# Performance work log

Hardware: AMD Instinct MI355X
Metric: run time of the kernel (lower is better)

The kernel has to match this reference:

```python
import jax, jax.numpy as jnp
import numpy as np

DIM = 768
NUM_HEADS = 12
HEAD_DIM = DIM // NUM_HEADS


def setup_inputs() -> dict:
    key = jax.random.key(0)
    k1, k2, k3 = jax.random.split(key, 3)
    B, N = 2, 2048
    x = jax.random.normal(k1, (B, N, DIM), dtype=jnp.float32)
    qkv_w = jax.random.normal(k2, (3 * DIM, DIM), dtype=jnp.float32) * 0.02
    proj_w = jax.random.normal(k3, (DIM, DIM), dtype=jnp.float32) * 0.02
    proj_b = jnp.zeros((DIM,), dtype=jnp.float32)
    freq_params = jnp.ones((NUM_HEADS, 1), dtype=jnp.float32) * 0.5  # Parameter init ones*0.5
    return {"x": x, "qkv_w": qkv_w, "proj_w": proj_w, "proj_b": proj_b,
            "freq_params": freq_params}


def _forward(x, qkv_w, proj_w, proj_b, freq_params):
    B, N, C = x.shape
    H, D = NUM_HEADS, HEAD_DIM
    scale = D ** (-0.5)
    # qkv projection -> (3, B, H, N, D)
    qkv = (x @ qkv_w.T).reshape(B, N, 3, H, D).transpose(2, 0, 3, 1, 4)
    q, k, v = qkv[0], qkv[1], qkv[2]
    # FFT along the token axis (axis=2 of [B,H,N,D])
    q_freq = jnp.fft.fft(q, axis=2)
    k_freq = jnp.fft.fft(k, axis=2)
    # Adaptive per-head low-pass: cutoff = int(N * sigmoid(freq_param)),
    # frequencies >= cutoff attenuated by exp(-(i - cutoff) / (N/4)).
    cutoff = jnp.floor(N * jax.nn.sigmoid(freq_params[:, 0]))        # (H,)
    idx = jnp.arange(N, dtype=jnp.float32)                            # (N,)
    rel = idx[None, :] - cutoff[:, None]                              # (H, N)
    atten = jnp.where(rel >= 0, jnp.exp(-rel / (N / 4.0)), 1.0)       # (H, N)
    atten = atten[None, :, :, None]                                   # (1, H, N, 1)
    q_filt = jnp.fft.ifft(q_freq * atten, axis=2).real
    k_filt = jnp.fft.ifft(k_freq * atten, axis=2).real
    # Attention
    attn = jnp.einsum('bhnd,bhmd->bhnm', q_filt, k_filt) * scale
    attn = jax.nn.softmax(attn, axis=-1)
    out = jnp.einsum('bhnm,bhmd->bhnd', attn, v)
    out = out.transpose(0, 2, 1, 3).reshape(B, N, C)
    return out @ proj_w.T + proj_b


def reference(x, qkv_w, proj_w, proj_b, freq_params):
    return _forward(x, qkv_w, proj_w, proj_b, freq_params)
```

## Files before the change

kernel.cpp:

```cpp
#include <hip/hip_runtime.h>
#include <math.h>

#define SEQ 2048
#define NH 12
#define HD 64
#define DIM 768

typedef _Float16 half_t;
typedef _Float16 f16x8 __attribute__((ext_vector_type(8)));
typedef _Float16 f16x4 __attribute__((ext_vector_type(4)));
typedef float f32x4 __attribute__((ext_vector_type(4)));

__device__ __forceinline__ void dma16(const half_t* g, half_t* l) {
  __builtin_amdgcn_global_load_lds(
      (const __attribute__((address_space(1))) unsigned int*)g,
      (__attribute__((address_space(3))) unsigned int*)l, 16, 0, 0);
}

__global__ __launch_bounds__(256) void cvt_f32_f16(
    const float* __restrict__ a, const float* __restrict__ b,
    const float* __restrict__ c, half_t* __restrict__ a16,
    half_t* __restrict__ b16, half_t* __restrict__ c16) {
  const size_t NA = 786432, NB = 442368;
  size_t i = (size_t)blockIdx.x * 256 + threadIdx.x;
  const float* src; half_t* dst; size_t off;
  if (i < NA) { src = a; dst = a16; off = i; }
  else if (i < NA + NB) { src = b; dst = b16; off = i - NA; }
  else { src = c; dst = c16; off = i - NA - NB; }
  float4 v = *(const float4*)&src[off * 4];
  f16x4 h;
  h[0] = (half_t)v.x; h[1] = (half_t)v.y; h[2] = (half_t)v.z; h[3] = (half_t)v.w;
  *(f16x4*)&dst[off * 4] = h;
}

__global__ __launch_bounds__(256) void gemm_qkv_f16(
    const half_t* __restrict__ x, const half_t* __restrict__ w,
    float* __restrict__ qT, float* __restrict__ kT, half_t* __restrict__ vb) {
  __shared__ half_t As[128][64];
  __shared__ half_t Bs[128][64];
  const int tid = threadIdx.x;
  const int lane = tid & 63, wave = tid >> 6;
  const int quad = lane >> 4, l16 = lane & 15;
  const int wr = wave >> 1, wc = wave & 1;
  const int row0 = blockIdx.y * 128;
  const int col0 = blockIdx.x * 128;
  const int srow = tid >> 3;
  const int schk = tid & 7;

  f32x4 acc[4][4] = {};

  for (int k0 = 0; k0 < DIM; k0 += 64) {
    f16x8 av[4], bv[4];
#pragma unroll
    for (int p = 0; p < 4; p++) {
      av[p] = *(const f16x8*)&x[(size_t)(row0 + srow + p * 32) * DIM + k0 + schk * 8];
      bv[p] = *(const f16x8*)&w[(size_t)(col0 + srow + p * 32) * DIM + k0 + schk * 8];
    }
    __syncthreads();
#pragma unroll
    for (int p = 0; p < 4; p++) {
      int r = srow + p * 32;
      int cs = ((schk ^ (r & 7)) << 3);
      *(f16x8*)&As[r][cs] = av[p];
      *(f16x8*)&Bs[r][cs] = bv[p];
    }
    __syncthreads();
#pragma unroll
    for (int ks = 0; ks < 2; ks++) {
      f16x8 af[4], bf[4];
#pragma unroll
      for (int i = 0; i < 4; i++) {
        int rr = wr * 64 + i * 16 + l16;
        af[i] = *(const f16x8*)&As[rr][((ks * 4 + quad) ^ (rr & 7)) << 3];
      }
#pragma unroll
      for (int j = 0; j < 4; j++) {
        int rr = wc * 64 + j * 16 + l16;
        bf[j] = *(const f16x8*)&Bs[rr][((ks * 4 + quad) ^ (rr & 7)) << 3];
      }
#pragma unroll
      for (int i = 0; i < 4; i++)
#pragma unroll
        for (int j = 0; j < 4; j++)
          acc[i][j] = __builtin_amdgcn_mfma_f32_16x16x32_f16(af[i], bf[j], acc[i][j], 0, 0, 0);
    }
  }

  const int fbase = col0 + wc * 64;
#pragma unroll
  for (int i = 0; i < 4; i++) {
    int n = row0 + wr * 64 + i * 16 + quad * 4;
    int b = n >> 11, nn = n & (SEQ - 1);
#pragma unroll
    for (int j = 0; j < 4; j++) {
      int f = fbase + j * 16 + l16;
      if (col0 < 1536) {
        float* dst = (col0 < 768) ? qT : kT;
        int fo = (col0 < 768) ? f : f - 768;
        *(f32x4*)&dst[((size_t)(b * 768 + fo)) * SEQ + nn] = acc[i][j];
      } else {
        int fo = f - 1536;
        int h = fo >> 6, d = fo & 63;
        int bh = b * NH + h;
        int ch = nn >> 6, cw = (nn & 63) >> 3, sub = nn & 7;
        f16x4 hv;
#pragma unroll
        for (int r = 0; r < 4; r++) hv[r] = (half_t)acc[i][j][r];
        *(f16x4*)&vb[((((size_t)bh * 32 + ch) * 64 + d) << 6) +
                     (((cw ^ (d & 7)) << 3) + sub)] = hv;
      }
    }
  }
}

__device__ __forceinline__ void fft2048_dif_fwd(float* re, float* im, int tid) {
  for (int M = 2048; M >= 8; M >>= 2) {
    const int q = M >> 2;
    const float ang = -6.283185307179586f / (float)M;
#pragma unroll 2
    for (int g = tid; g < 512; g += 256) {
      int j = g & (q - 1);
      int base = ((g & ~(q - 1)) << 2) | j;
      float s1, c1;
      __sincosf(ang * (float)j, &s1, &c1);
      float c2 = c1 * c1 - s1 * s1, s2 = 2.0f * c1 * s1;
      float Ar = re[base],         Ai = im[base];
      float Br = re[base + q],     Bi = im[base + q];
      float Cr = re[base + 2*q],   Ci = im[base + 2*q];
      float Dr = re[base + 3*q],   Di = im[base + 3*q];
      float A1r = Ar + Cr, A1i = Ai + Ci;
      float t1r = Ar - Cr, t1i = Ai - Ci;
      float C1r = c1 * t1r - s1 * t1i, C1i = c1 * t1i + s1 * t1r;
      float B1r = Br + Dr, B1i = Bi + Di;
      float t2r = Br - Dr, t2i = Bi - Di;
      float u2r = c1 * t2r - s1 * t2i, u2i = c1 * t2i + s1 * t2r;
      float D1r = u2i, D1i = -u2r;
      re[base]         = A1r + B1r; im[base]         = A1i + B1i;
      float t3r = A1r - B1r, t3i = A1i - B1i;
      re[base + q]     = c2 * t3r - s2 * t3i;
      im[base + q]     = c2 * t3i + s2 * t3r;
      re[base + 2*q]   = C1r + D1r; im[base + 2*q]   = C1i + D1i;
      float t4r = C1r - D1r, t4i = C1i - D1i;
      re[base + 3*q]   = c2 * t4r - s2 * t4i;
      im[base + 3*q]   = c2 * t4i + s2 * t4r;
    }
    __syncthreads();
  }
#pragma unroll 2
  for (int i = tid; i < 1024; i += 256) {
    float ar = re[2*i], ai = im[2*i], br = re[2*i+1], bi = im[2*i+1];
    re[2*i]   = ar + br; im[2*i]   = ai + bi;
    re[2*i+1] = ar - br; im[2*i+1] = ai - bi;
  }
  __syncthreads();
}

__device__ __forceinline__ void fft2048_dit_inv(float* re, float* im, int tid) {
  for (int L = 2; L <= 512; L <<= 2) {
    const int h = L >> 1;
    const float ang = 3.14159265358979f / (float)L;
#pragma unroll 2
    for (int g = tid; g < SEQ / 4; g += 256) {
      int p = g & (h - 1);
      int i0 = ((g & ~(h - 1)) << 2) | p;
      float s2, c2;
      __sincosf(ang * (float)p, &s2, &c2);
      float c1 = c2 * c2 - s2 * s2, s1 = 2.0f * c2 * s2;
      float ar = re[i0],         ai = im[i0];
      float br = re[i0 + h],     bi = im[i0 + h];
      float cr = re[i0 + L],     ci = im[i0 + L];
      float dr = re[i0 + L + h], di = im[i0 + L + h];
      float t1r = c1 * br - s1 * bi, t1i = c1 * bi + s1 * br;
      float a1r = ar + t1r, a1i = ai + t1i;
      float b1r = ar - t1r, b1i = ai - t1i;
      float t2r = c1 * dr - s1 * di, t2i = c1 * di + s1 * dr;
      float e1r = cr + t2r, e1i = ci + t2i;
      float d1r = cr - t2r, d1i = ci - t2i;
      float ur = c2 * e1r - s2 * e1i, ui = c2 * e1i + s2 * e1r;
      float vr = c2 * d1r - s2 * d1i, vi = c2 * d1i + s2 * d1r;
      float wr = -vi, wi = vr;
      re[i0]         = a1r + ur; im[i0]         = a1i + ui;
      re[i0 + L]     = a1r - ur; im[i0 + L]     = a1i - ui;
      re[i0 + h]     = b1r + wr; im[i0 + h]     = b1i + wi;
      re[i0 + L + h] = b1r - wr; im[i0 + L + h] = b1i - wi;
    }
    __syncthreads();
  }
  {
    const float ang = 6.283185307179586f / 2048.0f;
#pragma unroll 2
    for (int j = tid; j < 1024; j += 256) {
      float s, c;
      __sincosf(ang * (float)j, &s, &c);
      float x0r = re[j], x0i = im[j], x1r = re[j + 1024], x1i = im[j + 1024];
      float tr = c * x1r - s * x1i, ti = c * x1i + s * x1r;
      re[j] = x0r + tr;        im[j] = x0i + ti;
      re[j + 1024] = x0r - tr; im[j + 1024] = x0i - ti;
    }
    __syncthreads();
  }
}

__global__ __launch_bounds__(256) void fft_filter(
    const float* __restrict__ qT, const float* __restrict__ kT,
    half_t* __restrict__ qh, half_t* __restrict__ kh,
    const float* __restrict__ freq_params) {
  __shared__ float re[SEQ];
  __shared__ float im[SEQ];
  const int tid = threadIdx.x;
  const int idx = blockIdx.x;
  const int h = (idx >> 6) % NH;
  const float* qrow = qT + (size_t)idx * SEQ;
  const float* krow = kT + (size_t)idx * SEQ;

  for (int n = tid; n < SEQ; n += 256) { re[n] = qrow[n]; im[n] = krow[n]; }
  __syncthreads();
  fft2048_dif_fwd(re, im, tid);

  const float fp = freq_params[h];
  const float sig = 1.0f / (1.0f + expf(-fp));
  const float cutoff = floorf((float)SEQ * sig);

#pragma unroll 2
  for (int p = tid; p < SEQ; p += 256) {
    int n = (int)(__brev((unsigned)p) >> 21);
    int m = (SEQ - n) & (SEQ - 1);
    float r1 = (float)n - cutoff;
    float r2 = (float)m - cutoff;
    float A1 = (r1 >= 0.0f) ? __expf(-r1 * (1.0f / 512.0f)) : 1.0f;
    float A2 = (r2 >= 0.0f) ? __expf(-r2 * (1.0f / 512.0f)) : 1.0f;
    float Ae = 0.5f * (A1 + A2);
    re[p] *= Ae; im[p] *= Ae;
  }
  __syncthreads();

  fft2048_dit_inv(re, im, tid);

  const float inv = 1.0f / (float)SEQ;
  half_t* qo = qh + (size_t)idx * SEQ;
  half_t* ko = kh + (size_t)idx * SEQ;
  for (int n = tid; n < SEQ; n += 256) {
    qo[n] = (half_t)(re[n] * inv);
    ko[n] = (half_t)(im[n] * inv);
  }
}

__global__ __launch_bounds__(256) void transpose_qk16(
    const half_t* __restrict__ qh, const half_t* __restrict__ kh,
    half_t* __restrict__ qA, half_t* __restrict__ kA) {
  __shared__ half_t tl[64][65];
  const int swz = blockIdx.z;
  const half_t* src = swz ? kh : qh;
  half_t* dst = swz ? kA : qA;
  const int t = threadIdx.x;
  const int N0 = blockIdx.x * 64;
  const int bh = blockIdx.y;
#pragma unroll
  for (int i = 0; i < 2; i++) {
    int idx = i * 256 + t;
    int d = idx >> 3, n8 = (idx & 7) << 3;
    f16x8 v = *(const f16x8*)&src[((size_t)(bh * 64 + d)) * SEQ + N0 + n8];
#pragma unroll
    for (int j = 0; j < 8; j++) tl[d][n8 + j] = v[j];
  }
  __syncthreads();
#pragma unroll
  for (int i = 0; i < 2; i++) {
    int idx = i * 256 + t;
    int nl = idx >> 3, chunk = idx & 7;
    f16x8 v;
#pragma unroll
    for (int j = 0; j < 8; j++) v[j] = tl[chunk * 8 + j][nl];
    int cs = swz ? (chunk ^ (nl & 7)) : chunk;
    *(f16x8*)&dst[((size_t)(bh * SEQ + N0 + nl)) * 64 + cs * 8] = v;
  }
}

__global__ __launch_bounds__(256) void attention_v6(
    const half_t* __restrict__ qA, const half_t* __restrict__ kA,
    const half_t* __restrict__ vb, float* __restrict__ part0,
    float* __restrict__ part1, float* __restrict__ Lp0,
    float* __restrict__ Lp1) {
  __shared__ half_t ks[2][64][64];
  __shared__ half_t vs[2][64][64];
  const int t = threadIdx.x;
  const int lane = t & 63, wave = t >> 6;
  const int quad = lane >> 4, l16 = lane & 15;
  const int id = blockIdx.x;
  const int bh = (id & 7) * 3 + ((id >> 3) % 3);
  const int rest = id / 24;
  const int qt = rest >> 1, mh = rest & 1;
  const int N0 = qt * 128;
  float* part = mh ? part1 : part0;
  float* Lp = mh ? Lp1 : Lp0;
  const half_t* kbase = kA + ((size_t)bh * SEQ + mh * 1024) * 64;
  const half_t* vbase = vb + (((size_t)bh * 32 + mh * 16) << 12);

  f16x8 qlo[2], qhi[2];
#pragma unroll
  for (int u = 0; u < 2; u++) {
    int n = N0 + wave * 32 + u * 16 + l16;
    const half_t* qp = qA + ((size_t)bh * SEQ + n) * 64;
    qlo[u] = *(const f16x8*)(qp + quad * 8);
    qhi[u] = *(const f16x8*)(qp + 32 + quad * 8);
  }

#pragma unroll
  for (int i = 0; i < 2; i++) {
    int ins = wave * 2 + i;
    dma16(kbase + ins * 512 + lane * 8, &ks[0][ins * 8][0]);
    dma16(vbase + ins * 512 + lane * 8, &vs[0][ins * 8][0]);
  }

  f32x4 acc[2][4] = {};
  float Ls[2] = {0.0f, 0.0f};
  const float SC = 0.18033688011112042f;
  const float SH = -2.8853900817779268f;

  for (int c = 0; c < 16; c++) {
    const int cur = c & 1;
    __syncthreads();

    const int cn = (c < 15) ? c + 1 : 0;
#pragma unroll
    for (int i = 0; i < 2; i++) {
      int ins = wave * 2 + i;
      dma16(kbase + (size_t)cn * 4096 + ins * 512 + lane * 8,
            &ks[1 - cur][ins * 8][0]);
      dma16(vbase + (size_t)cn * 4096 + ins * 512 + lane * 8,
            &vs[1 - cur][ins * 8][0]);
    }

    f16x4 pf[2][4];
#pragma unroll
    for (int j = 0; j < 4; j++) {
      int row = j * 16 + l16;
      int sw = row & 7;
      f16x8 klo = *(const f16x8*)&ks[cur][row][(quad ^ sw) * 8];
      f16x8 khi = *(const f16x8*)&ks[cur][row][((quad + 4) ^ sw) * 8];
#pragma unroll
      for (int u = 0; u < 2; u++) {
        f32x4 s = {};
        s = __builtin_amdgcn_mfma_f32_16x16x32_f16(klo, qlo[u], s, 0, 0, 0);
        s = __builtin_amdgcn_mfma_f32_16x16x32_f16(khi, qhi[u], s, 0, 0, 0);
#pragma unroll
        for (int r = 0; r < 4; r++) {
          float p = exp2f(fmaf(s[r], SC, SH));
          Ls[u] += p;
          pf[u][j][r] = (half_t)p;
        }
      }
    }

#pragma unroll
    for (int j = 0; j < 4; j++)
#pragma unroll
      for (int dt = 0; dt < 4; dt++) {
        int d = dt * 16 + l16;
        int cc = ((2 * j + (quad >> 1)) ^ (d & 7));
        f16x4 bv = *(const f16x4*)&vs[cur][d][cc * 8 + (quad & 1) * 4];
        acc[0][dt] = __builtin_amdgcn_mfma_f32_16x16x16f16(pf[0][j], bv, acc[0][dt], 0, 0, 0);
        acc[1][dt] = __builtin_amdgcn_mfma_f32_16x16x16f16(pf[1][j], bv, acc[1][dt], 0, 0, 0);
      }
  }

#pragma unroll
  for (int u = 0; u < 2; u++) {
    float L = Ls[u];
    L += __shfl_xor(L, 16, 64);
    L += __shfl_xor(L, 32, 64);
    if (quad == 0) Lp[(size_t)bh * SEQ + N0 + wave * 32 + u * 16 + l16] = L;
#pragma unroll
    for (int dt = 0; dt < 4; dt++) {
#pragma unroll
      for (int r = 0; r < 4; r++) {
        int n = N0 + wave * 32 + u * 16 + quad * 4 + r;
        part[((size_t)bh * SEQ + n) * 64 + dt * 16 + l16] = acc[u][dt][r];
      }
    }
  }
}

__global__ __launch_bounds__(256) void combine_o(
    const float* __restrict__ p0, const float* __restrict__ p1,
    const float* __restrict__ L0, const float* __restrict__ L1,
    half_t* __restrict__ ao) {
  int idx = blockIdx.x * 256 + threadIdx.x;
  int row = idx >> 4;
  int d = (idx & 15) << 2;
  f32x4 a = *(const f32x4*)&p0[(size_t)row * 64 + d];
  f32x4 b = *(const f32x4*)&p1[(size_t)row * 64 + d];
  float inv = 1.0f / (L0[row] + L1[row]);
  int bh = row >> 11, n = row & (SEQ - 1);
  int bb = bh / NH, h = bh % NH;
  f16x4 o;
#pragma unroll
  for (int r = 0; r < 4; r++) o[r] = (half_t)((a[r] + b[r]) * inv);
  *(f16x4*)&ao[((size_t)(bb * SEQ + n)) * DIM + h * 64 + d] = o;
}

__global__ __launch_bounds__(256) void gemm_proj_f16(
    const half_t* __restrict__ ao, const half_t* __restrict__ w,
    const float* __restrict__ bias, float* __restrict__ out) {
  __shared__ half_t As[128][64];
  __shared__ half_t Bs[128][64];
  const int tid = threadIdx.x;
  const int lane = tid & 63, wave = tid >> 6;
  const int quad = lane >> 4, l16 = lane & 15;
  const int wr = wave >> 1, wc = wave & 1;
  const int row0 = blockIdx.y * 128;
  const int col0 = blockIdx.x * 128;
  const int srow = tid >> 3;
  const int schk = tid & 7;

  f32x4 acc[4][4] = {};

  for (int k0 = 0; k0 < DIM; k0 += 64) {
    f16x8 av[4], bv[4];
#pragma unroll
    for (int p = 0; p < 4; p++) {
      av[p] = *(const f16x8*)&ao[(size_t)(row0 + srow + p * 32) * DIM + k0 + schk * 8];
      bv[p] = *(const f16x8*)&w[(size_t)(col0 + srow + p * 32) * DIM + k0 + schk * 8];
    }
    __syncthreads();
#pragma unroll
    for (int p = 0; p < 4; p++) {
      int r = srow + p * 32;
      int cs = ((schk ^ (r & 7)) << 3);
      *(f16x8*)&As[r][cs] = av[p];
      *(f16x8*)&Bs[r][cs] = bv[p];
    }
    __syncthreads();
#pragma unroll
    for (int ks = 0; ks < 2; ks++) {
      f16x8 af[4], bf[4];
#pragma unroll
      for (int i = 0; i < 4; i++) {
        int rr = wr * 64 + i * 16 + l16;
        af[i] = *(const f16x8*)&As[rr][((ks * 4 + quad) ^ (rr & 7)) << 3];
      }
#pragma unroll
      for (int j = 0; j < 4; j++) {
        int rr = wc * 64 + j * 16 + l16;
        bf[j] = *(const f16x8*)&Bs[rr][((ks * 4 + quad) ^ (rr & 7)) << 3];
      }
#pragma unroll
      for (int i = 0; i < 4; i++)
#pragma unroll
        for (int j = 0; j < 4; j++)
          acc[i][j] = __builtin_amdgcn_mfma_f32_16x16x32_f16(af[i], bf[j], acc[i][j], 0, 0, 0);
    }
  }

#pragma unroll
  for (int i = 0; i < 4; i++) {
    int m = row0 + wr * 64 + i * 16 + quad * 4;
#pragma unroll
    for (int j = 0; j < 4; j++) {
      int f = col0 + wc * 64 + j * 16 + l16;
      float bj = bias[f];
#pragma unroll
      for (int r = 0; r < 4; r++)
        out[(size_t)(m + r) * DIM + f] = acc[i][j][r] + bj;
    }
  }
}

extern "C" void kernel_launch(void* const* d_in, const int* in_sizes, int n_in,
                              void* d_out, int out_size, void* d_ws, size_t ws_size,
                              hipStream_t stream) {
  (void)in_sizes; (void)n_in; (void)out_size; (void)ws_size;
  const float* x      = (const float*)d_in[0];
  const float* qkv_w  = (const float*)d_in[1];
  const float* proj_w = (const float*)d_in[2];
  const float* proj_b = (const float*)d_in[3];
  const float* freq   = (const float*)d_in[4];
  float* out = (float*)d_out;
  char* ws = (char*)d_ws;

  half_t* wp16 = (half_t*)(ws);
  float*  qT   = (float*)(ws + 1179648);
  float*  kT   = (float*)(ws + 13762560);
  half_t* v_b  = (half_t*)(ws + 26345472);
  half_t* x16  = (half_t*)(ws + 32636928);
  half_t* w16  = (half_t*)(ws + 38928384);
  half_t* q_h  = (half_t*)(ws + 42467328);
  half_t* k_h  = (half_t*)(ws + 32636928);
  float*  part0 = (float*)(ws + 1179648);
  float*  part1 = (float*)(ws + 13762560);
  float*  Lp0  = (float*)(ws + 38928384);
  float*  Lp1  = (float*)(ws + 38928384 + 196608);
  half_t* ao   = (half_t*)(ws + 42467328);
  half_t* qA   = (half_t*)d_out;
  half_t* kA   = (half_t*)((char*)d_out + 6291456);

  cvt_f32_f16<<<5376, 256, 0, stream>>>(x, qkv_w, proj_w, x16, w16, wp16);
  gemm_qkv_f16<<<dim3(18, 32), 256, 0, stream>>>(x16, w16, qT, kT, v_b);
  fft_filter<<<1536, 256, 0, stream>>>(qT, kT, q_h, k_h, freq);
  transpose_qk16<<<dim3(32, 24, 2), 256, 0, stream>>>(q_h, k_h, qA, kA);
  attention_v6<<<768, 256, 0, stream>>>(qA, kA, v_b, part0, part1, Lp0, Lp1);
  combine_o<<<3072, 256, 0, stream>>>(part0, part1, Lp0, Lp1, ao);
  gemm_proj_f16<<<dim3(6, 32), 256, 0, stream>>>(ao, wp16, proj_b, out);
}
```

Measured before the change: 216.2 us.

## Pre-swizzle GEMM inputs, use async LDS DMA, drop Q transpose, MFMA row sums

The conversion kernel now writes x and qkv_w in an XOR-swizzled layout, so the QKV GEMM can stream tiles into double-buffered LDS with global_load_lds DMA instead of staging through registers with two barriers per step. The Q transpose is removed and attention gathers Q straight from the [d][n] FFT output with strided scalar loads. Softmax row sums are now taken with an extra MFMA against a ones vector instead of scalar adds plus shuffles. The gains are one fewer pass over Q and less register/barrier overhead, at the cost of uncoalesced Q loads and more MFMA work per tile.

New measurement: 211.7 us. 2.1% less time.

```diff
diff --git a/kernel.cpp b/kernel.cpp
--- a/kernel.cpp
+++ b/kernel.cpp
@@ -23,60 +23,74 @@
     half_t* __restrict__ b16, half_t* __restrict__ c16) {
   const size_t NA = 786432, NB = 442368;
   size_t i = (size_t)blockIdx.x * 256 + threadIdx.x;
-  const float* src; half_t* dst; size_t off;
-  if (i < NA) { src = a; dst = a16; off = i; }
-  else if (i < NA + NB) { src = b; dst = b16; off = i - NA; }
-  else { src = c; dst = c16; off = i - NA - NB; }
-  float4 v = *(const float4*)&src[off * 4];
-  f16x4 h;
-  h[0] = (half_t)v.x; h[1] = (half_t)v.y; h[2] = (half_t)v.z; h[3] = (half_t)v.w;
-  *(f16x4*)&dst[off * 4] = h;
+  if (i < NA + NB) {
+    const float* src = (i < NA) ? a : b;
+    half_t* dst = (i < NA) ? a16 : b16;
+    size_t off = (i < NA) ? i : i - NA;
+    float4 v = *(const float4*)&src[off * 4];
+    f16x4 h;
+    h[0] = (half_t)v.x; h[1] = (half_t)v.y; h[2] = (half_t)v.z; h[3] = (half_t)v.w;
+    int row = (int)((off * 4) / DIM);
+    int col = (int)((off * 4) % DIM);
+    int sc = col ^ ((row & 7) << 3);
+    *(f16x4*)&dst[(size_t)row * DIM + sc] = h;
+  } else {
+    size_t off = i - NA - NB;
+    float4 v = *(const float4*)&c[off * 4];
+    f16x4 h;
+    h[0] = (half_t)v.x; h[1] = (half_t)v.y; h[2] = (half_t)v.z; h[3] = (half_t)v.w;
+    *(f16x4*)&c16[off * 4] = h;
+  }
 }
 
 __global__ __launch_bounds__(256) void gemm_qkv_f16(
-    const half_t* __restrict__ x, const half_t* __restrict__ w,
+    const half_t* __restrict__ xs, const half_t* __restrict__ ws,
     float* __restrict__ qT, float* __restrict__ kT, half_t* __restrict__ vb) {
-  __shared__ half_t As[128][64];
-  __shared__ half_t Bs[128][64];
+  __shared__ half_t As[2][128][64];
+  __shared__ half_t Bs[2][128][64];
   const int tid = threadIdx.x;
   const int lane = tid & 63, wave = tid >> 6;
   const int quad = lane >> 4, l16 = lane & 15;
   const int wr = wave >> 1, wc = wave & 1;
   const int row0 = blockIdx.y * 128;
   const int col0 = blockIdx.x * 128;
-  const int srow = tid >> 3;
-  const int schk = tid & 7;
+  const int rl = lane >> 3, ch = lane & 7;
+
+#pragma unroll
+  for (int i = 0; i < 4; i++) {
+    int ins = wave * 4 + i;
+    dma16(xs + (size_t)(row0 + ins * 8 + rl) * DIM + ch * 8, &As[0][ins * 8][0]);
+    dma16(ws + (size_t)(col0 + ins * 8 + rl) * DIM + ch * 8, &Bs[0][ins * 8][0]);
+  }
 
   f32x4 acc[4][4] = {};
 
-  for (int k0 = 0; k0 < DIM; k0 += 64) {
-    f16x8 av[4], bv[4];
-#pragma unroll
-    for (int p = 0; p < 4; p++) {
-      av[p] = *(const f16x8*)&x[(size_t)(row0 + srow + p * 32) * DIM + k0 + schk * 8];
-      bv[p] = *(const f16x8*)&w[(size_t)(col0 + srow + p * 32) * DIM + k0 + schk * 8];
-    }
-    __syncthreads();
-#pragma unroll
-    for (int p = 0; p < 4; p++) {
-      int r = srow + p * 32;
-      int cs = ((schk ^ (r & 7)) << 3);
-      *(f16x8*)&As[r][cs] = av[p];
-      *(f16x8*)&Bs[r][cs] = bv[p];
-    }
-    __syncthreads();
+  for (int c = 0; c < 12; c++) {
+    const int cur = c & 1;
+    __syncthreads();
+    if (c < 11) {
+      int k0 = (c + 1) * 64;
+#pragma unroll
+      for (int i = 0; i < 4; i++) {
+        int ins = wave * 4 + i;
+        dma16(xs + (size_t)(row0 + ins * 8 + rl) * DIM + k0 + ch * 8,
+              &As[1 - cur][ins * 8][0]);
+        dma16(ws + (size_t)(col0 + ins * 8 + rl) * DIM + k0 + ch * 8,
+              &Bs[1 - cur][ins * 8][0]);
+      }
+    }
 #pragma unroll
     for (int ks = 0; ks < 2; ks++) {
       f16x8 af[4], bf[4];
 #pragma unroll
       for (int i = 0; i < 4; i++) {
         int rr = wr * 64 + i * 16 + l16;
-        af[i] = *(const f16x8*)&As[rr][((ks * 4 + quad) ^ (rr & 7)) << 3];
+        af[i] = *(const f16x8*)&As[cur][rr][((ks * 4 + quad) ^ (rr & 7)) << 3];
       }
 #pragma unroll
       for (int j = 0; j < 4; j++) {
         int rr = wc * 64 + j * 16 + l16;
-        bf[j] = *(const f16x8*)&Bs[rr][((ks * 4 + quad) ^ (rr & 7)) << 3];
+        bf[j] = *(const f16x8*)&Bs[cur][rr][((ks * 4 + quad) ^ (rr & 7)) << 3];
       }
 #pragma unroll
       for (int i = 0; i < 4; i++)
@@ -102,11 +116,11 @@
         int fo = f - 1536;
         int h = fo >> 6, d = fo & 63;
         int bh = b * NH + h;
-        int ch = nn >> 6, cw = (nn & 63) >> 3, sub = nn & 7;
+        int chn = nn >> 6, cw = (nn & 63) >> 3, sub = nn & 7;
         f16x4 hv;
 #pragma unroll
         for (int r = 0; r < 4; r++) hv[r] = (half_t)acc[i][j][r];
-        *(f16x4*)&vb[((((size_t)bh * 32 + ch) * 64 + d) << 6) +
+        *(f16x4*)&vb[((((size_t)bh * 32 + chn) * 64 + d) << 6) +
                      (((cw ^ (d & 7)) << 3) + sub)] = hv;
       }
     }
@@ -245,13 +259,9 @@
   }
 }
 
-__global__ __launch_bounds__(256) void transpose_qk16(
-    const half_t* __restrict__ qh, const half_t* __restrict__ kh,
-    half_t* __restrict__ qA, half_t* __restrict__ kA) {
+__global__ __launch_bounds__(256) void transpose_k16(
+    const half_t* __restrict__ kh, half_t* __restrict__ kA) {
   __shared__ half_t tl[64][65];
-  const int swz = blockIdx.z;
-  const half_t* src = swz ? kh : qh;
-  half_t* dst = swz ? kA : qA;
   const int t = threadIdx.x;
   const int N0 = blockIdx.x * 64;
   const int bh = blockIdx.y;
@@ -259,7 +269,7 @@
   for (int i = 0; i < 2; i++) {
     int idx = i * 256 + t;
     int d = idx >> 3, n8 = (idx & 7) << 3;
-    f16x8 v = *(const f16x8*)&src[((size_t)(bh * 64 + d)) * SEQ + N0 + n8];
+    f16x8 v = *(const f16x8*)&kh[((size_t)(bh * 64 + d)) * SEQ + N0 + n8];
 #pragma unroll
     for (int j = 0; j < 8; j++) tl[d][n8 + j] = v[j];
   }
@@ -271,13 +281,12 @@
     f16x8 v;
 #pragma unroll
     for (int j = 0; j < 8; j++) v[j] = tl[chunk * 8 + j][nl];
-    int cs = swz ? (chunk ^ (nl & 7)) : chunk;
-    *(f16x8*)&dst[((size_t)(bh * SEQ + N0 + nl)) * 64 + cs * 8] = v;
-  }
-}
-
-__global__ __launch_bounds__(256) void attention_v6(
-    const half_t* __restrict__ qA, const half_t* __restrict__ kA,
+    *(f16x8*)&kA[((size_t)(bh * SEQ + N0 + nl)) * 64 + (chunk ^ (nl & 7)) * 8] = v;
+  }
+}
+
+__global__ __launch_bounds__(256) void attention_v7(
+    const half_t* __restrict__ q_h, const half_t* __restrict__ kA,
     const half_t* __restrict__ vb, float* __restrict__ part0,
     float* __restrict__ part1, float* __restrict__ Lp0,
     float* __restrict__ Lp1) {
@@ -295,14 +304,17 @@
   float* Lp = mh ? Lp1 : Lp0;
   const half_t* kbase = kA + ((size_t)bh * SEQ + mh * 1024) * 64;
   const half_t* vbase = vb + (((size_t)bh * 32 + mh * 16) << 12);
+  const half_t* qb = q_h + (size_t)bh * 64 * SEQ;
 
   f16x8 qlo[2], qhi[2];
 #pragma unroll
   for (int u = 0; u < 2; u++) {
     int n = N0 + wave * 32 + u * 16 + l16;
-    const half_t* qp = qA + ((size_t)bh * SEQ + n) * 64;
-    qlo[u] = *(const f16x8*)(qp + quad * 8);
-    qhi[u] = *(const f16x8*)(qp + 32 + quad * 8);
+#pragma unroll
+    for (int e = 0; e < 8; e++) {
+      qlo[u][e] = qb[(size_t)(quad * 8 + e) * SEQ + n];
+      qhi[u][e] = qb[(size_t)(32 + quad * 8 + e) * SEQ + n];
+    }
   }
 
 #pragma unroll
@@ -313,7 +325,10 @@
   }
 
   f32x4 acc[2][4] = {};
-  float Ls[2] = {0.0f, 0.0f};
+  f32x4 accL[2] = {};
+  f16x4 ones;
+  ones[0] = (half_t)1.0f; ones[1] = (half_t)1.0f;
+  ones[2] = (half_t)1.0f; ones[3] = (half_t)1.0f;
   const float SC = 0.18033688011112042f;
   const float SH = -2.8853900817779268f;
 
@@ -344,16 +359,15 @@
         s = __builtin_amdgcn_mfma_f32_16x16x32_f16(klo, qlo[u], s, 0, 0, 0);
         s = __builtin_amdgcn_mfma_f32_16x16x32_f16(khi, qhi[u], s, 0, 0, 0);
 #pragma unroll
-        for (int r = 0; r < 4; r++) {
-          float p = exp2f(fmaf(s[r], SC, SH));
-          Ls[u] += p;
-          pf[u][j][r] = (half_t)p;
-        }
-      }
-    }
-
-#pragma unroll
-    for (int j = 0; j < 4; j++)
+        for (int r = 0; r < 4; r++)
+          pf[u][j][r] = (half_t)exp2f(fmaf(s[r], SC, SH));
+      }
+    }
+
+#pragma unroll
+    for (int j = 0; j < 4; j++) {
+      accL[0] = __builtin_amdgcn_mfma_f32_16x16x16f16(pf[0][j], ones, accL[0], 0, 0, 0);
+      accL[1] = __builtin_amdgcn_mfma_f32_16x16x16f16(pf[1][j], ones, accL[1], 0, 0, 0);
 #pragma unroll
       for (int dt = 0; dt < 4; dt++) {
         int d = dt * 16 + l16;
@@ -362,14 +376,16 @@
         acc[0][dt] = __builtin_amdgcn_mfma_f32_16x16x16f16(pf[0][j], bv, acc[0][dt], 0, 0, 0);
         acc[1][dt] = __builtin_amdgcn_mfma_f32_16x16x16f16(pf[1][j], bv, acc[1][dt], 0, 0, 0);
       }
+    }
   }
 
 #pragma unroll
   for (int u = 0; u < 2; u++) {
-    float L = Ls[u];
-    L += __shfl_xor(L, 16, 64);
-    L += __shfl_xor(L, 32, 64);
-    if (quad == 0) Lp[(size_t)bh * SEQ + N0 + wave * 32 + u * 16 + l16] = L;
+    if (l16 == 0) {
+#pragma unroll
+      for (int r = 0; r < 4; r++)
+        Lp[(size_t)bh * SEQ + N0 + wave * 32 + u * 16 + quad * 4 + r] = accL[u][r];
+    }
 #pragma unroll
     for (int dt = 0; dt < 4; dt++) {
 #pragma unroll
@@ -491,14 +507,13 @@
   float*  Lp0  = (float*)(ws + 38928384);
   float*  Lp1  = (float*)(ws + 38928384 + 196608);
   half_t* ao   = (half_t*)(ws + 42467328);
-  half_t* qA   = (half_t*)d_out;
-  half_t* kA   = (half_t*)((char*)d_out + 6291456);
+  half_t* kA   = (half_t*)d_out;
 
   cvt_f32_f16<<<5376, 256, 0, stream>>>(x, qkv_w, proj_w, x16, w16, wp16);
   gemm_qkv_f16<<<dim3(18, 32), 256, 0, stream>>>(x16, w16, qT, kT, v_b);
   fft_filter<<<1536, 256, 0, stream>>>(qT, kT, q_h, k_h, freq);
-  transpose_qk16<<<dim3(32, 24, 2), 256, 0, stream>>>(q_h, k_h, qA, kA);
-  attention_v6<<<768, 256, 0, stream>>>(qA, kA, v_b, part0, part1, Lp0, Lp1);
+  transpose_k16<<<dim3(32, 24), 256, 0, stream>>>(k_h, kA);
+  attention_v7<<<768, 256, 0, stream>>>(q_h, kA, v_b, part0, part1, Lp0, Lp1);
   combine_o<<<3072, 256, 0, stream>>>(part0, part1, Lp0, Lp1, ao);
   gemm_proj_f16<<<dim3(6, 32), 256, 0, stream>>>(ao, wp16, proj_b, out);
 }
```
